# Kernel tuning notes

Hardware: AMD Instinct MI355X
Metric: run time of the kernel (lower is better)

## Reference

```python
import jax, jax.numpy as jnp
import numpy as np

K = 10  # num_neighbors in original nn_index call


def setup_inputs() -> dict:
    key = jax.random.key(0)
    k1, k2, k3, k4 = jax.random.split(key, 4)
    B, OBS, ACT, N = 256, 32, 2, 500000
    obs = jax.random.normal(k1, (B, OBS), dtype=jnp.float32)
    action = jax.random.normal(k2, (B, ACT), dtype=jnp.float32)
    mem_sa = jax.random.normal(k3, (N, OBS + ACT), dtype=jnp.float32)
    mem_Q = jax.random.normal(k4, (N, 1), dtype=jnp.float32)
    return {"obs": obs, "action": action, "mem_sa": mem_sa, "mem_Q": mem_Q}


def reference(obs, action, mem_sa, mem_Q):
    # query: [B, D] state-action, brute-force kNN over memory table [N, D]
    q = jnp.concatenate([obs, action], axis=1)
    # squared Euclidean distances (FLANN returns squared L2): [B, N]
    d2 = (jnp.sum(q * q, axis=1, keepdims=True)
          - 2.0 * q @ mem_sa.T
          + jnp.sum(mem_sa * mem_sa, axis=1)[None, :])
    neg_d, idx = jax.lax.top_k(-d2, K)   # nearest K neighbors
    dists = -neg_d                        # [B, K], ascending
    Qs = mem_Q[idx, 0]                    # gather Q values: [B, K]
    # NOTE: original applies softmax to raw distances (not negated)
    weights = jax.nn.softmax(dists, axis=1)
    return jnp.sum(weights * Qs, axis=1)  # [B]
```

## Files before the change

### kernel.cpp

```cpp
#include <hip/hip_runtime.h>
#include <hip/hip_bf16.h>
#include <math.h>

#define NPTS   500000
#define NB     256
#define TOPK   10
#define CAP    2048
#define SBLK   1024
#define SPER   16
#define MARGIN 2.0f
#define FPTS   128
#define NCHUNK 3907
#define FBLK   1536
#define LCAP   8
#define MS     40
#define PMAIN  393216
#define OCAP   32768

typedef short v4s  __attribute__((ext_vector_type(4)));
typedef short v8s  __attribute__((ext_vector_type(8)));
typedef float v16f __attribute__((ext_vector_type(16)));

__device__ __forceinline__ unsigned short f2bf(float f) {
    unsigned u = __float_as_uint(f);
    unsigned r = u + 0x7FFFu + ((u >> 16) & 1u);
    return (unsigned short)(r >> 16);
}
__device__ __forceinline__ float bf2f(unsigned short h) {
    return __uint_as_float(((unsigned)h) << 16);
}

__device__ __forceinline__ float norm34(const float* __restrict__ r) {
    float a0 = 0.f, a1 = 0.f, a2 = 0.f, a3 = 0.f;
#pragma unroll
    for (int d = 0; d < 32; d += 4) {
        a0 = fmaf(r[d + 0], r[d + 0], a0);
        a1 = fmaf(r[d + 1], r[d + 1], a1);
        a2 = fmaf(r[d + 2], r[d + 2], a2);
        a3 = fmaf(r[d + 3], r[d + 3], a3);
    }
    a0 = fmaf(r[32], r[32], a0);
    a1 = fmaf(r[33], r[33], a1);
    return (a0 + a1) + (a2 + a3);
}
__device__ __forceinline__ float dot34(const float* __restrict__ r, const float* q) {
    float a0 = 0.f, a1 = 0.f, a2 = 0.f, a3 = 0.f;
#pragma unroll
    for (int d = 0; d < 32; d += 4) {
        a0 = fmaf(r[d + 0], q[d + 0], a0);
        a1 = fmaf(r[d + 1], q[d + 1], a1);
        a2 = fmaf(r[d + 2], q[d + 2], a2);
        a3 = fmaf(r[d + 3], q[d + 3], a3);
    }
    a0 = fmaf(r[32], q[32], a0);
    a1 = fmaf(r[33], q[33], a1);
    return (a0 + a1) + (a2 + a3);
}
__device__ __forceinline__ float dot34_v4(const float4* __restrict__ r4, const float* q) {
    float a0 = 0.f, a1 = 0.f, a2 = 0.f, a3 = 0.f;
#pragma unroll
    for (int dp = 0; dp < 8; ++dp) {
        float4 v = r4[dp];
        a0 = fmaf(v.x, q[4 * dp + 0], a0);
        a1 = fmaf(v.y, q[4 * dp + 1], a1);
        a2 = fmaf(v.z, q[4 * dp + 2], a2);
        a3 = fmaf(v.w, q[4 * dp + 3], a3);
    }
    float2 t = *(const float2*)(r4 + 8);
    a0 = fmaf(t.x, q[32], a0);
    a1 = fmaf(t.y, q[33], a1);
    return (a0 + a1) + (a2 + a3);
}
__device__ __forceinline__ void load_q(const float* __restrict__ obs,
                                       const float* __restrict__ act, int b, float* q) {
#pragma unroll
    for (int d = 0; d < 32; ++d) q[d] = obs[b * 32 + d];
    q[32] = act[b * 2 + 0];
    q[33] = act[b * 2 + 1];
}

__global__ __launch_bounds__(256, 4) void k_sample(const float* __restrict__ obs,
                                                   const float* __restrict__ act,
                                                   const float* __restrict__ msa,
                                                   float* __restrict__ minima) {
    __shared__ __align__(16) float sm[SPER * 36];
    __shared__ float smn[SPER];
    const int g = blockIdx.x, t = threadIdx.x;
    const int base = g * SPER;
    for (int i = t; i < SPER * 34; i += 256) {
        int row = i / 34, d = i - row * 34;
        sm[row * 36 + d] = msa[(size_t)base * 34 + i];
    }
    __syncthreads();
    if (t < SPER) smn[t] = norm34(&sm[t * 36]);
    __syncthreads();
    float q[34];
    load_q(obs, act, t, q);
    float best = __builtin_inff();
#pragma unroll
    for (int j = 0; j < SPER; ++j) {
        float s = fmaf(-2.f, dot34_v4((const float4*)&sm[j * 36], q), smn[j]);
        best = fminf(best, s);
    }
    minima[(size_t)t * SBLK + g] = best;
}

__global__ __launch_bounds__(64) void k_tau(const float* __restrict__ minima,
                                            const float* __restrict__ obs,
                                            const float* __restrict__ act,
                                            v8s* __restrict__ afrag,
                                            int* __restrict__ cursor) {
    __shared__ __align__(16) unsigned short qs[48];
    const int b = blockIdx.x, lane = threadIdx.x;
    if (b == 0 && lane == 0) { cursor[0] = 0; cursor[1] = 0; }
    float v[16];
#pragma unroll
    for (int k = 0; k < 16; ++k) v[k] = minima[(size_t)b * SBLK + lane + 64 * k];
    float last = 0.f;
    for (int r = 0; r < TOPK; ++r) {
        float lm = v[0]; int la = 0;
#pragma unroll
        for (int k = 1; k < 16; ++k) { if (v[k] < lm) { lm = v[k]; la = k; } }
        float wm = lm;
        for (int off = 32; off; off >>= 1) wm = fminf(wm, __shfl_xor(wm, off));
        unsigned long long msk = __ballot(lm == wm);
        int first = (int)__builtin_ctzll(msk);
        if (lane == first) {
#pragma unroll
            for (int k = 0; k < 16; ++k) { if (k == la) v[k] = __builtin_inff(); }
        }
        last = wm;
    }
    float val = 0.f;
    if (lane < 32)       val = obs[b * 32 + lane];
    else if (lane < 34)  val = act[b * 2 + (lane - 32)];
    else if (lane == 34) val = -0.5f;
    else if (lane == 35) val = 0.5f * (last + MARGIN);
    if (lane < 48) qs[lane] = (lane < 36) ? f2bf(val) : (unsigned short)0;
    __syncthreads();
    if (lane < 6) {
        int s = lane >> 1, half = lane & 1;
        int qt = b >> 5, mrow = b & 31;
        v8s frag = *(const v8s*)&qs[s * 16 + half * 8];
        afrag[(qt * 3 + s) * 64 + half * 32 + mrow] = frag;
    }
}

__global__ __launch_bounds__(256, 6) void k_filter(const float* __restrict__ msa,
                                                   const v8s* __restrict__ afrag,
                                                   int* __restrict__ cursor,
                                                   unsigned* __restrict__ pbuf,
                                                   int* __restrict__ posq) {
    __shared__ __align__(16) unsigned short lm[FPTS * MS];
    __shared__ int lcount[NB];
    __shared__ int lcand[NB * LCAP];
    __shared__ int gbase;
    const int g = blockIdx.x, t = threadIdx.x;
    const int w = t >> 6, lane = t & 63;
    const int mrow = lane & 31, half = lane >> 5;
    lcount[t] = 0;
#pragma unroll 1
    for (int rep = 0; rep < 3; ++rep) {
        const int c = g + rep * FBLK;
        if (c >= NCHUNK) break;
        const int lo = c * FPTS;
        __syncthreads();
        for (int i = t; i < FPTS * 17; i += 256) {
            int row = i / 17, dp = i - row * 17;
            int gp = lo + row;
            float2 v = make_float2(0.f, 0.f);
            if (gp < NPTS) v = *(const float2*)&msa[(size_t)gp * 34 + 2 * dp];
            __hip_bfloat162 h2 = __float22bfloat162_rn(v);
            unsigned pk;
            __builtin_memcpy(&pk, &h2, 4);
            *(unsigned*)&lm[row * MS + 2 * dp] = pk;
        }
        __syncthreads();
        const unsigned short* myrow = &lm[(w * 32 + mrow) * MS];
        const int p0 = lo + w * 32 + mrow;
        float n0 = 0.f, n1 = 0.f, n2 = 0.f, n3 = 0.f;
#pragma unroll
        for (int dq = 0; dq < 4; ++dq) {
            v4s h4 = *(const v4s*)(myrow + 4 * dq);
            float f0 = bf2f((unsigned short)h4[0]);
            float f1 = bf2f((unsigned short)h4[1]);
            float f2 = bf2f((unsigned short)h4[2]);
            float f3 = bf2f((unsigned short)h4[3]);
            n0 = fmaf(f0, f0, n0);
            n1 = fmaf(f1, f1, n1);
            n2 = fmaf(f2, f2, n2);
            n3 = fmaf(f3, f3, n3);
        }
#pragma unroll
        for (int dq = 4; dq < 8; ++dq) {
            v4s h4 = *(const v4s*)(myrow + 4 * dq);
            float f0 = bf2f((unsigned short)h4[0]);
            float f1 = bf2f((unsigned short)h4[1]);
            float f2 = bf2f((unsigned short)h4[2]);
            float f3 = bf2f((unsigned short)h4[3]);
            n0 = fmaf(f0, f0, n0);
            n1 = fmaf(f1, f1, n1);
            n2 = fmaf(f2, f2, n2);
            n3 = fmaf(f3, f3, n3);
        }
        unsigned u33 = *(const unsigned*)(myrow + 32);
        {
            float f0 = bf2f((unsigned short)(u33 & 0xFFFFu));
            float f1 = bf2f((unsigned short)(u33 >> 16));
            n0 = fmaf(f0, f0, n0);
            n1 = fmaf(f1, f1, n1);
        }
        float thr = 0.5f * ((n0 + n1) + (n2 + n3));
        if (p0 >= NPTS) thr = 1e30f;
        const v8s B0 = *(const v8s*)(myrow + half * 8);
        const v8s B1 = *(const v8s*)(myrow + 16 + half * 8);
        v8s B2 = (v8s)(short)0;
        if (half == 0) {
            B2[0] = (short)(unsigned short)(u33 & 0xFFFFu);
            B2[1] = (short)(unsigned short)(u33 >> 16);
            B2[3] = (short)0x3F80;
        }
#pragma unroll 1
        for (int qt = 0; qt < 8; ++qt) {
            v8s A0 = afrag[(qt * 3 + 0) * 64 + lane];
            v8s A1 = afrag[(qt * 3 + 1) * 64 + lane];
            v8s A2 = afrag[(qt * 3 + 2) * 64 + lane];
            v16f acc;
#pragma unroll
            for (int i = 0; i < 16; ++i) acc[i] = 0.f;
            acc = __builtin_amdgcn_mfma_f32_32x32x16_bf16(A0, B0, acc, 0, 0, 0);
            acc = __builtin_amdgcn_mfma_f32_32x32x16_bf16(A1, B1, acc, 0, 0, 0);
            acc = __builtin_amdgcn_mfma_f32_32x32x16_bf16(A2, B2, acc, 0, 0, 0);
            unsigned hm = 0;
#pragma unroll
            for (int r = 0; r < 16; ++r) hm |= (acc[r] >= thr) ? (1u << r) : 0u;
            while (hm) {
                int r = __builtin_ctz(hm);
                hm &= hm - 1;
                int qq = qt * 32 + (r & 3) + 8 * (r >> 2) + 4 * half;
                int slot = atomicAdd(&lcount[qq], 1);
                if (slot < LCAP) lcand[qq * LCAP + slot] = p0;
                else {
                    int dg = atomicAdd(cursor + 1, 1);
                    if (dg < OCAP) pbuf[PMAIN + dg] = ((unsigned)qq << 19) | (unsigned)p0;
                }
            }
        }
    }
    __syncthreads();
    int n = lcount[t];
    if (n > LCAP) n = LCAP;
    lcount[t] = n;
    __syncthreads();
    for (int off = 1; off < 256; off <<= 1) {
        int v = (t >= off) ? lcount[t - off] : 0;
        __syncthreads();
        lcount[t] += v;
        __syncthreads();
    }
    int base_l = lcount[t] - n;
    if (t == 255) gbase = atomicAdd(cursor, lcount[255]);
    __syncthreads();
    int start = gbase + base_l;
    if (start >= PMAIN) { start = 0; n = 0; }
    else if (start + n > PMAIN) n = PMAIN - start;
    posq[g * NB + t] = start | (n << 20);
    for (int i = 0; i < n; ++i)
        pbuf[start + i] = (unsigned)lcand[t * LCAP + i];
}

__global__ __launch_bounds__(256) void k_final(const float* __restrict__ obs,
                                               const float* __restrict__ act,
                                               const float* __restrict__ msa,
                                               const unsigned* __restrict__ pbuf,
                                               const int* __restrict__ posq,
                                               const int* __restrict__ cursor,
                                               const float* __restrict__ memQ,
                                               float* __restrict__ out) {
    __shared__ float ls[CAP];
    __shared__ int   li[CAP];
    __shared__ int   sc[NB];
    __shared__ int   lcnt;
    __shared__ float rs[4];
    __shared__ int   ri[4];
    __shared__ float sel_s[TOPK];
    __shared__ int   sel_i[TOPK];
    const int b = blockIdx.x, t = threadIdx.x;
    const int lane = t & 63, wid = t >> 6;
    int nk[6], pk6[6], tot = 0;
#pragma unroll
    for (int k = 0; k < 6; ++k) {
        int packed = posq[(size_t)(t + 256 * k) * NB + b];
        nk[k] = (packed >> 20) & 0xF;
        pk6[k] = packed & 0xFFFFF;
        tot += nk[k];
    }
    sc[t] = tot;
    __syncthreads();
    for (int off = 1; off < 256; off <<= 1) {
        int v = (t >= off) ? sc[t - off] : 0;
        __syncthreads();
        sc[t] += v;
        __syncthreads();
    }
    int myoff = sc[t] - tot;
    if (t == 0) lcnt = (sc[255] > CAP) ? CAP : sc[255];
    __syncthreads();
#pragma unroll
    for (int k = 0; k < 6; ++k)
        for (int i = 0; i < nk[k]; ++i) {
            if (myoff < CAP) li[myoff] = (int)pbuf[pk6[k] + i];
            ++myoff;
        }
    int novf = cursor[1];
    if (novf > OCAP) novf = OCAP;
    for (int j = t; j < novf; j += 256) {
        unsigned pr = pbuf[PMAIN + j];
        if ((int)(pr >> 19) == b) {
            int s = atomicAdd(&lcnt, 1);
            if (s < CAP) li[s] = (int)(pr & 0x7FFFFu);
        }
    }
    __syncthreads();
    int cnt = lcnt;
    if (cnt > CAP) cnt = CAP;
    float q[34];
    load_q(obs, act, b, q);
    for (int j = t; j < cnt; j += 256) {
        const float* row = msa + (size_t)li[j] * 34;
        ls[j] = fmaf(-2.f, dot34(row, q), norm34(row));
    }
    __syncthreads();
    for (int k = 0; k < TOPK; ++k) {
        float bs = __builtin_inff();
        int   bi = 0x7fffffff;
        for (int j = t; j < cnt; j += 256) {
            float s = ls[j]; int i = li[j];
            if (s < bs || (s == bs && i < bi)) { bs = s; bi = i; }
        }
        for (int off = 32; off; off >>= 1) {
            float s2 = __shfl_down(bs, off);
            int   i2 = __shfl_down(bi, off);
            if (s2 < bs || (s2 == bs && i2 < bi)) { bs = s2; bi = i2; }
        }
        if (lane == 0) { rs[wid] = bs; ri[wid] = bi; }
        __syncthreads();
        if (t == 0) {
            float fs = rs[0]; int fi = ri[0];
#pragma unroll
            for (int ww = 1; ww < 4; ++ww) {
                if (rs[ww] < fs || (rs[ww] == fs && ri[ww] < fi)) { fs = rs[ww]; fi = ri[ww]; }
            }
            sel_s[k] = fs; sel_i[k] = fi;
        }
        __syncthreads();
        const int win = sel_i[k];
        for (int j = t; j < cnt; j += 256) {
            if (li[j] == win) ls[j] = __builtin_inff();
        }
        __syncthreads();
    }
    if (t == 0) {
        float m = sel_s[TOPK - 1];
        float wsum = 0.f, acc = 0.f;
#pragma unroll
        for (int k = 0; k < TOPK; ++k) {
            if (sel_i[k] == 0x7fffffff) continue;
            float w2 = expf(sel_s[k] - m);
            wsum += w2;
            acc = fmaf(w2, memQ[sel_i[k]], acc);
        }
        out[b] = acc / wsum;
    }
}

extern "C" void kernel_launch(void* const* d_in, const int* in_sizes, int n_in,
                              void* d_out, int out_size, void* d_ws, size_t ws_size,
                              hipStream_t stream) {
    const float* obs = (const float*)d_in[0];
    const float* act = (const float*)d_in[1];
    const float* msa = (const float*)d_in[2];
    const float* mq  = (const float*)d_in[3];
    float* out = (float*)d_out;

    char* ws = (char*)d_ws;
    int*      cursor = (int*)ws;
    v8s*      afrag  = (v8s*)(ws + 256);
    float*    minima = (float*)(ws + 32768);
    int*      posq   = (int*)(ws + 32768 + 1048576);
    unsigned* pbuf   = (unsigned*)(ws + 32768 + 1048576 + 1572864);

    k_sample<<<SBLK, 256, 0, stream>>>(obs, act, msa, minima);
    k_tau   <<<NB, 64, 0, stream>>>(minima, obs, act, afrag, cursor);
    k_filter<<<FBLK, 256, 0, stream>>>(msa, afrag, cursor, pbuf, posq);
    k_final <<<NB, 256, 0, stream>>>(obs, act, msa, pbuf, posq, cursor, mq, out);
}
```

Before: 187.3 us.

## Load filter MFMA operands straight from global memory, drop LDS staging

The filter kernel no longer stages 128-point chunks into shared memory as bf16. Each wavefront now loads its 32 points' float2 elements directly from global memory into registers and packs them into the MFMA B fragments itself. Each point's norm is computed in fp32 as two partial sums, one per half of the wave, combined with a cross-lane shuffle. This removes the LDS round trip, two block barriers per chunk and the shared-memory footprint, which may also raise occupancy. The cost is uncoalesced, strided 8-byte global loads, and the threshold now uses fp32 rather than bf16-rounded norms.

```diff
diff --git a/kernel.cpp b/kernel.cpp
--- a/kernel.cpp
+++ b/kernel.cpp
@@ -9,14 +9,13 @@
 #define SBLK   1024
 #define SPER   16
 #define MARGIN 2.0f
-#define FPTS   128
-#define NCHUNK 3907
+#define NWCH   15625
 #define FBLK   1536
 #define LCAP   8
-#define MS     40
 #define PMAIN  393216
 #define OCAP   32768
 
+typedef short v2s  __attribute__((ext_vector_type(2)));
 typedef short v4s  __attribute__((ext_vector_type(4)));
 typedef short v8s  __attribute__((ext_vector_type(8)));
 typedef float v16f __attribute__((ext_vector_type(16)));
@@ -28,6 +27,12 @@
 }
 __device__ __forceinline__ float bf2f(unsigned short h) {
     return __uint_as_float(((unsigned)h) << 16);
+}
+__device__ __forceinline__ v2s pk2(float2 f) {
+    __hip_bfloat162 h = __float22bfloat162_rn(f);
+    v2s r;
+    __builtin_memcpy(&r, &h, 4);
+    return r;
 }
 
 __device__ __forceinline__ float norm34(const float* __restrict__ r) {
@@ -151,7 +156,6 @@
                                                    int* __restrict__ cursor,
                                                    unsigned* __restrict__ pbuf,
                                                    int* __restrict__ posq) {
-    __shared__ __align__(16) unsigned short lm[FPTS * MS];
     __shared__ int lcount[NB];
     __shared__ int lcand[NB * LCAP];
     __shared__ int gbase;
@@ -159,65 +163,46 @@
     const int w = t >> 6, lane = t & 63;
     const int mrow = lane & 31, half = lane >> 5;
     lcount[t] = 0;
+    __syncthreads();
+    const int gw = g * 4 + w;
 #pragma unroll 1
-    for (int rep = 0; rep < 3; ++rep) {
-        const int c = g + rep * FBLK;
-        if (c >= NCHUNK) break;
-        const int lo = c * FPTS;
-        __syncthreads();
-        for (int i = t; i < FPTS * 17; i += 256) {
-            int row = i / 17, dp = i - row * 17;
-            int gp = lo + row;
-            float2 v = make_float2(0.f, 0.f);
-            if (gp < NPTS) v = *(const float2*)&msa[(size_t)gp * 34 + 2 * dp];
-            __hip_bfloat162 h2 = __float22bfloat162_rn(v);
-            unsigned pk;
-            __builtin_memcpy(&pk, &h2, 4);
-            *(unsigned*)&lm[row * MS + 2 * dp] = pk;
-        }
-        __syncthreads();
-        const unsigned short* myrow = &lm[(w * 32 + mrow) * MS];
-        const int p0 = lo + w * 32 + mrow;
-        float n0 = 0.f, n1 = 0.f, n2 = 0.f, n3 = 0.f;
-#pragma unroll
-        for (int dq = 0; dq < 4; ++dq) {
-            v4s h4 = *(const v4s*)(myrow + 4 * dq);
-            float f0 = bf2f((unsigned short)h4[0]);
-            float f1 = bf2f((unsigned short)h4[1]);
-            float f2 = bf2f((unsigned short)h4[2]);
-            float f3 = bf2f((unsigned short)h4[3]);
-            n0 = fmaf(f0, f0, n0);
-            n1 = fmaf(f1, f1, n1);
-            n2 = fmaf(f2, f2, n2);
-            n3 = fmaf(f3, f3, n3);
-        }
-#pragma unroll
-        for (int dq = 4; dq < 8; ++dq) {
-            v4s h4 = *(const v4s*)(myrow + 4 * dq);
-            float f0 = bf2f((unsigned short)h4[0]);
-            float f1 = bf2f((unsigned short)h4[1]);
-            float f2 = bf2f((unsigned short)h4[2]);
-            float f3 = bf2f((unsigned short)h4[3]);
-            n0 = fmaf(f0, f0, n0);
-            n1 = fmaf(f1, f1, n1);
-            n2 = fmaf(f2, f2, n2);
-            n3 = fmaf(f3, f3, n3);
-        }
-        unsigned u33 = *(const unsigned*)(myrow + 32);
-        {
-            float f0 = bf2f((unsigned short)(u33 & 0xFFFFu));
-            float f1 = bf2f((unsigned short)(u33 >> 16));
-            n0 = fmaf(f0, f0, n0);
-            n1 = fmaf(f1, f1, n1);
-        }
-        float thr = 0.5f * ((n0 + n1) + (n2 + n3));
-        if (p0 >= NPTS) thr = 1e30f;
-        const v8s B0 = *(const v8s*)(myrow + half * 8);
-        const v8s B1 = *(const v8s*)(myrow + 16 + half * 8);
+    for (int wc = gw; wc < NWCH; wc += FBLK * 4) {
+        const int p0 = wc * 32 + mrow;
+        const float* rp = msa + (size_t)p0 * 34;
+        float2 e0 = *(const float2*)(rp + half * 8 + 0);
+        float2 e1 = *(const float2*)(rp + half * 8 + 2);
+        float2 e2 = *(const float2*)(rp + half * 8 + 4);
+        float2 e3 = *(const float2*)(rp + half * 8 + 6);
+        float2 e4 = *(const float2*)(rp + 16 + half * 8 + 0);
+        float2 e5 = *(const float2*)(rp + 16 + half * 8 + 2);
+        float2 e6 = *(const float2*)(rp + 16 + half * 8 + 4);
+        float2 e7 = *(const float2*)(rp + 16 + half * 8 + 6);
+        float2 e8 = *(const float2*)(rp + 32);
+        float n0 = 0.f, n1 = 0.f;
+        n0 = fmaf(e0.x, e0.x, n0); n1 = fmaf(e0.y, e0.y, n1);
+        n0 = fmaf(e1.x, e1.x, n0); n1 = fmaf(e1.y, e1.y, n1);
+        n0 = fmaf(e2.x, e2.x, n0); n1 = fmaf(e2.y, e2.y, n1);
+        n0 = fmaf(e3.x, e3.x, n0); n1 = fmaf(e3.y, e3.y, n1);
+        n0 = fmaf(e4.x, e4.x, n0); n1 = fmaf(e4.y, e4.y, n1);
+        n0 = fmaf(e5.x, e5.x, n0); n1 = fmaf(e5.y, e5.y, n1);
+        n0 = fmaf(e6.x, e6.x, n0); n1 = fmaf(e6.y, e6.y, n1);
+        n0 = fmaf(e7.x, e7.x, n0); n1 = fmaf(e7.y, e7.y, n1);
+        float part = n0 + n1;
+        part = fmaf(e8.x, e8.x * 0.5f, part);
+        part = fmaf(e8.y, e8.y * 0.5f, part);
+        float nrm = part + __shfl_xor(part, 32);
+        float thr = 0.5f * nrm;
+        v4s b0lo = __builtin_shufflevector(pk2(e0), pk2(e1), 0, 1, 2, 3);
+        v4s b0hi = __builtin_shufflevector(pk2(e2), pk2(e3), 0, 1, 2, 3);
+        v8s B0 = __builtin_shufflevector(b0lo, b0hi, 0, 1, 2, 3, 4, 5, 6, 7);
+        v4s b1lo = __builtin_shufflevector(pk2(e4), pk2(e5), 0, 1, 2, 3);
+        v4s b1hi = __builtin_shufflevector(pk2(e6), pk2(e7), 0, 1, 2, 3);
+        v8s B1 = __builtin_shufflevector(b1lo, b1hi, 0, 1, 2, 3, 4, 5, 6, 7);
         v8s B2 = (v8s)(short)0;
         if (half == 0) {
-            B2[0] = (short)(unsigned short)(u33 & 0xFFFFu);
-            B2[1] = (short)(unsigned short)(u33 >> 16);
+            v2s m33 = pk2(e8);
+            B2[0] = m33[0];
+            B2[1] = m33[1];
             B2[3] = (short)0x3F80;
         }
 #pragma unroll 1
```

After: 182.3 us. -2.6%, faster.
